# Performance work log

Measured on AMD Instinct MI355X. Metric: run time of the kernel, lower is better.

The kernel has to match this reference:

```python
import jax, jax.numpy as jnp
import numpy as np

N, C, L, NUM_LAYERS = 512, 32, 1024, 3
BN_EPS = 1e-5


def setup_inputs() -> dict:
    key = jax.random.key(0)
    kx, kw, kb, kg, kbe = jax.random.split(key, 5)
    x = jax.random.normal(kx, (N, C, L), dtype=jnp.float32)
    # Per-channel, per-layer Linear weights: (C, num_layers, L_out, L_in)
    W = jax.random.normal(kw, (C, NUM_LAYERS, L, L), dtype=jnp.float32) / np.float32(np.sqrt(L))
    b = 0.01 * jax.random.normal(kb, (C, NUM_LAYERS, L), dtype=jnp.float32)
    # BatchNorm affine params for the num_layers-1 inner BN layers
    gamma = 1.0 + 0.1 * jax.random.normal(kg, (C, NUM_LAYERS - 1, L), dtype=jnp.float32)
    beta = 0.1 * jax.random.normal(kbe, (C, NUM_LAYERS - 1, L), dtype=jnp.float32)
    return {"x": x, "W": W, "b": b, "gamma": gamma, "beta": beta}


def reference(x, W, b, gamma, beta):
    """Fused per-channel MLP head.

    x: (N, C, L). For each channel c, applies num_layers Linear layers with
    ReLU + BatchNorm1d (training-mode batch stats, biased variance) between
    layers. All C channels computed as one batched GEMM per layer.
    """
    h = x
    for i in range(NUM_LAYERS):
        # batched per-channel Linear: (N,C,Lin) x (C,Lout,Lin) -> (N,C,Lout)
        h = jnp.einsum('ncl,cml->ncm', h, W[:, i]) + b[:, i][None]
        if i < NUM_LAYERS - 1:
            h = jax.nn.relu(h)
            # BatchNorm1d over the batch dim N, per (channel, feature)
            mean = jnp.mean(h, axis=0)          # (C, L)
            var = jnp.var(h, axis=0)            # biased variance, matches torch BN
            h = (h - mean) * jax.lax.rsqrt(var + BN_EPS) * gamma[:, i] + beta[:, i]
    return h
```

## Files before the change

kernel.cpp:

```cpp
#include <hip/hip_runtime.h>
#include <hip/hip_bf16.h>

#define NB 512
#define CCH 32
#define LF 1024
#define CL (CCH * LF)
#define BN_EPS 1e-5f

typedef __bf16 bf16x8 __attribute__((ext_vector_type(8)));
typedef __bf16 bf16x4 __attribute__((ext_vector_type(4)));
typedef float f32x4 __attribute__((ext_vector_type(4)));

__device__ __forceinline__ void gload16(const void* g, void* l) {
  auto gp = (const __attribute__((address_space(1))) void*)(uintptr_t)g;
  auto lp = (__attribute__((address_space(3))) void*)(uint32_t)(uintptr_t)l;
  __builtin_amdgcn_global_load_lds(gp, lp, 16, 0, 0);
}

__global__ __launch_bounds__(256) void cvt_x(const float* __restrict__ x,
                                             __bf16* __restrict__ xb) {
  const int c = blockIdx.y;
  const int wv = threadIdx.x >> 6, lane = threadIdx.x & 63;
  const int n0 = blockIdx.x * 8;
#pragma unroll
  for (int rr = 0; rr < 2; ++rr) {
    const int n = n0 + wv * 2 + rr;
    const float* src = x + ((size_t)n * CCH + c) * LF;
    __bf16* dst = xb + ((size_t)c * NB + n) * LF;
#pragma unroll
    for (int j = 0; j < 4; ++j) {
      const int col = (j * 64 + lane) * 4;
      f32x4 v = *(const f32x4*)(src + col);
      bf16x4 o = {(__bf16)v.x, (__bf16)v.y, (__bf16)v.z, (__bf16)v.w};
      *(bf16x4*)(dst + col) = o;
    }
  }
}

template <bool HAS_BN>
__global__ __launch_bounds__(256) void fold_w(
    const float* __restrict__ Wall, const float* __restrict__ ball,
    const float* __restrict__ scale, const float* __restrict__ shift,
    __bf16* __restrict__ Wb, float* __restrict__ bout, int layer) {
  const int c = blockIdx.y;
  const int wv = threadIdx.x >> 6, lane = threadIdx.x & 63;
  const float* Wp = Wall + (size_t)(c * 3 + layer) * LF * LF;
  const float* scl = scale + (size_t)c * LF;
  const float* shf = shift + (size_t)c * LF;
  const int m0 = blockIdx.x * 16 + wv * 4;
#pragma unroll
  for (int rr = 0; rr < 4; ++rr) {
    const int m = m0 + rr;
    const float* wrow = Wp + (size_t)m * LF;
    __bf16* orow = Wb + (size_t)c * LF * LF + (size_t)m * LF;
    float dot = 0.f;
#pragma unroll
    for (int j = 0; j < 4; ++j) {
      const int col = (j * 64 + lane) * 4;
      f32x4 w = *(const f32x4*)(wrow + col);
      if (HAS_BN) {
        f32x4 s = *(const f32x4*)(scl + col);
        f32x4 t = *(const f32x4*)(shf + col);
        dot += w.x * t.x + w.y * t.y + w.z * t.z + w.w * t.w;
        f32x4 wsc = w * s;
        bf16x4 o = {(__bf16)wsc.x, (__bf16)wsc.y, (__bf16)wsc.z, (__bf16)wsc.w};
        *(bf16x4*)(orow + col) = o;
      } else {
        bf16x4 o = {(__bf16)w.x, (__bf16)w.y, (__bf16)w.z, (__bf16)w.w};
        *(bf16x4*)(orow + col) = o;
      }
    }
    if (HAS_BN) {
#pragma unroll
      for (int off = 32; off >= 1; off >>= 1) dot += __shfl_down(dot, off);
    }
    if (lane == 0)
      bout[(size_t)c * LF + m] =
          ball[(size_t)(c * 3 + layer) * LF + m] + (HAS_BN ? dot : 0.f);
  }
}

template <bool RELU, bool OUTBF>
__global__ __launch_bounds__(256, 2) void gemm_k(
    const __bf16* __restrict__ Ab, const __bf16* __restrict__ Wb,
    const float* __restrict__ bf, void* __restrict__ Out) {
  __shared__ __bf16 As[128 * 32];
  __shared__ __bf16 Bs[128 * 32];
  const int tid = threadIdx.x;
  const int c = blockIdx.y;
  const int mtile = blockIdx.x & 3;
  const int ntile = blockIdx.x >> 2;

  const int lane = tid & 63;
  const int wv = tid >> 6;
  const int wm = (wv & 1) * 64;
  const int wn = (wv >> 1) * 64;
  const int l15 = lane & 15;
  const int quad = lane >> 4;

  const int srow = lane >> 2;
  const int skel = (lane & 3) * 8;

  const __bf16* Ag = Ab + (size_t)c * NB * LF +
                     (size_t)(mtile * 128 + wv * 32 + srow) * LF + skel;
  const __bf16* Bg = Wb + (size_t)c * LF * LF +
                     (size_t)(ntile * 128 + wv * 32 + srow) * LF + skel;
  __bf16* Al = &As[(wv * 32) * 32];
  __bf16* Bl = &Bs[(wv * 32) * 32];

  f32x4 acc[4][4] = {};

  for (int kt = 0; kt < LF / 32; ++kt) {
    const int k0 = kt * 32;
    gload16(Ag + k0, Al);
    gload16(Ag + 16 * LF + k0, Al + 16 * 32);
    gload16(Bg + k0, Bl);
    gload16(Bg + 16 * LF + k0, Bl + 16 * 32);
    __syncthreads();

    bf16x8 af[4], bfr[4];
#pragma unroll
    for (int mi = 0; mi < 4; ++mi)
      af[mi] = *(const bf16x8*)&As[(wm + mi * 16 + l15) * 32 + quad * 8];
#pragma unroll
    for (int ni = 0; ni < 4; ++ni)
      bfr[ni] = *(const bf16x8*)&Bs[(wn + ni * 16 + l15) * 32 + quad * 8];
#pragma unroll
    for (int mi = 0; mi < 4; ++mi)
#pragma unroll
      for (int ni = 0; ni < 4; ++ni)
        acc[mi][ni] = __builtin_amdgcn_mfma_f32_16x16x32_bf16(
            af[mi], bfr[ni], acc[mi][ni], 0, 0, 0);
    __syncthreads();
  }

  const float* bias = bf + (size_t)c * LF;
  if (OUTBF) {
    __bf16* outp = (__bf16*)Out + (size_t)c * NB * LF;
#pragma unroll
    for (int ni = 0; ni < 4; ++ni) {
      const int feat = ntile * 128 + wn + ni * 16 + l15;
      const float bvv = bias[feat];
#pragma unroll
      for (int mi = 0; mi < 4; ++mi) {
        const int row0 = mtile * 128 + wm + mi * 16 + quad * 4;
#pragma unroll
        for (int r = 0; r < 4; ++r) {
          float v = acc[mi][ni][r] + bvv;
          if (RELU) v = fmaxf(v, 0.f);
          outp[(size_t)(row0 + r) * LF + feat] = (__bf16)v;
        }
      }
    }
  } else {
    float* outp = (float*)Out + (size_t)c * LF;
#pragma unroll
    for (int ni = 0; ni < 4; ++ni) {
      const int feat = ntile * 128 + wn + ni * 16 + l15;
      const float bvv = bias[feat];
#pragma unroll
      for (int mi = 0; mi < 4; ++mi) {
        const int row0 = mtile * 128 + wm + mi * 16 + quad * 4;
#pragma unroll
        for (int r = 0; r < 4; ++r) {
          float v = acc[mi][ni][r] + bvv;
          if (RELU) v = fmaxf(v, 0.f);
          outp[(size_t)(row0 + r) * CL + feat] = v;
        }
      }
    }
  }
}

__global__ __launch_bounds__(256) void bn_stats(
    const __bf16* __restrict__ H, const float* __restrict__ gamma,
    const float* __restrict__ beta, float* __restrict__ scale,
    float* __restrict__ shift, int bnlayer) {
  __shared__ float s_sum[256], s_sq[256];
  const int tid = threadIdx.x;
  const int f = tid & 63, g = tid >> 6;
  const int c = blockIdx.y;
  const int l = blockIdx.x * 64 + f;
  const __bf16* col = H + (size_t)c * NB * LF + l;
  float sum = 0.f, sq = 0.f;
  for (int n = g; n < NB; n += 4) {
    float v = (float)col[(size_t)n * LF];
    sum += v;
    sq += v * v;
  }
  s_sum[tid] = sum;
  s_sq[tid] = sq;
  __syncthreads();
  if (g == 0) {
    sum = s_sum[f] + s_sum[64 + f] + s_sum[128 + f] + s_sum[192 + f];
    sq = s_sq[f] + s_sq[64 + f] + s_sq[128 + f] + s_sq[192 + f];
    const float mean = sum * (1.f / NB);
    const float var = sq * (1.f / NB) - mean * mean;
    const float rstd = rsqrtf(var + BN_EPS);
    const float ga = gamma[(size_t)(c * 2 + bnlayer) * LF + l];
    const float be = beta[(size_t)(c * 2 + bnlayer) * LF + l];
    const float sc = rstd * ga;
    scale[(size_t)c * LF + l] = sc;
    shift[(size_t)c * LF + l] = be - mean * sc;
  }
}

extern "C" void kernel_launch(void* const* d_in, const int* in_sizes, int n_in,
                              void* d_out, int out_size, void* d_ws,
                              size_t ws_size, hipStream_t stream) {
  const float* x = (const float*)d_in[0];
  const float* W = (const float*)d_in[1];
  const float* b = (const float*)d_in[2];
  const float* gamma = (const float*)d_in[3];
  const float* beta = (const float*)d_in[4];
  float* out = (float*)d_out;

  char* ws = (char*)d_ws;
  float* scale = (float*)ws;  ws += (size_t)CL * 4;
  float* shift = (float*)ws;  ws += (size_t)CL * 4;
  float* bfold = (float*)ws;  ws += (size_t)CL * 4;
  __bf16* xb = (__bf16*)ws;   ws += (size_t)NB * CL * 2;
  __bf16* h1 = (__bf16*)ws;   ws += (size_t)NB * CL * 2;
  __bf16* h2 = (__bf16*)ws;   ws += (size_t)NB * CL * 2;
  __bf16* Wfold = (__bf16*)ws;

  const dim3 blk(256);
  const dim3 ggrid(32, 32);
  const dim3 fgrid(64, 32);
  const dim3 sgrid(16, 32);

  cvt_x<<<fgrid, blk, 0, stream>>>(x, xb);
  fold_w<false><<<fgrid, blk, 0, stream>>>(W, b, scale, shift, Wfold, bfold, 0);
  gemm_k<true, true><<<ggrid, blk, 0, stream>>>(xb, Wfold, bfold, h1);
  bn_stats<<<sgrid, blk, 0, stream>>>(h1, gamma, beta, scale, shift, 0);
  fold_w<true><<<fgrid, blk, 0, stream>>>(W, b, scale, shift, Wfold, bfold, 1);
  gemm_k<true, true><<<ggrid, blk, 0, stream>>>(h1, Wfold, bfold, h2);
  bn_stats<<<sgrid, blk, 0, stream>>>(h2, gamma, beta, scale, shift, 1);
  fold_w<true><<<fgrid, blk, 0, stream>>>(W, b, scale, shift, Wfold, bfold, 2);
  gemm_k<false, false><<<ggrid, blk, 0, stream>>>(h2, Wfold, bfold, out);
}
```

Measured before the change: 867.0 us.

## Apply BatchNorm to activations instead of folding it into weights; convert all weights once

Drops the per-layer weight folding, where BN scale and shift were baked into a bf16 copy of W along with a bias dot product. All three layers' weights are now converted to bf16 in one kernel up front, and BN stats plus normalization are applied directly to the activations, which adds an extra read and write of the activation buffer per layer. The GEMM grid is also remapped to a 1D index that interleaves channels, likely to improve cache locality. This trades the serialized fold-then-GEMM dependency for extra activation traffic and a large up-front weight conversion.

```diff
diff --git a/kernel.cpp b/kernel.cpp
--- a/kernel.cpp
+++ b/kernel.cpp
@@ -37,59 +37,40 @@
   }
 }
 
-template <bool HAS_BN>
-__global__ __launch_bounds__(256) void fold_w(
-    const float* __restrict__ Wall, const float* __restrict__ ball,
-    const float* __restrict__ scale, const float* __restrict__ shift,
-    __bf16* __restrict__ Wb, float* __restrict__ bout, int layer) {
-  const int c = blockIdx.y;
+__global__ __launch_bounds__(256) void cvt_w(const float* __restrict__ Wall,
+                                             __bf16* __restrict__ Wb) {
+  const int slab = blockIdx.y;
   const int wv = threadIdx.x >> 6, lane = threadIdx.x & 63;
-  const float* Wp = Wall + (size_t)(c * 3 + layer) * LF * LF;
-  const float* scl = scale + (size_t)c * LF;
-  const float* shf = shift + (size_t)c * LF;
+  const float* Wp = Wall + (size_t)slab * LF * LF;
+  __bf16* Op = Wb + (size_t)slab * LF * LF;
   const int m0 = blockIdx.x * 16 + wv * 4;
 #pragma unroll
   for (int rr = 0; rr < 4; ++rr) {
     const int m = m0 + rr;
     const float* wrow = Wp + (size_t)m * LF;
-    __bf16* orow = Wb + (size_t)c * LF * LF + (size_t)m * LF;
-    float dot = 0.f;
+    __bf16* orow = Op + (size_t)m * LF;
 #pragma unroll
     for (int j = 0; j < 4; ++j) {
       const int col = (j * 64 + lane) * 4;
       f32x4 w = *(const f32x4*)(wrow + col);
-      if (HAS_BN) {
-        f32x4 s = *(const f32x4*)(scl + col);
-        f32x4 t = *(const f32x4*)(shf + col);
-        dot += w.x * t.x + w.y * t.y + w.z * t.z + w.w * t.w;
-        f32x4 wsc = w * s;
-        bf16x4 o = {(__bf16)wsc.x, (__bf16)wsc.y, (__bf16)wsc.z, (__bf16)wsc.w};
-        *(bf16x4*)(orow + col) = o;
-      } else {
-        bf16x4 o = {(__bf16)w.x, (__bf16)w.y, (__bf16)w.z, (__bf16)w.w};
-        *(bf16x4*)(orow + col) = o;
-      }
-    }
-    if (HAS_BN) {
-#pragma unroll
-      for (int off = 32; off >= 1; off >>= 1) dot += __shfl_down(dot, off);
-    }
-    if (lane == 0)
-      bout[(size_t)c * LF + m] =
-          ball[(size_t)(c * 3 + layer) * LF + m] + (HAS_BN ? dot : 0.f);
+      bf16x4 o = {(__bf16)w.x, (__bf16)w.y, (__bf16)w.z, (__bf16)w.w};
+      *(bf16x4*)(orow + col) = o;
+    }
   }
 }
 
 template <bool RELU, bool OUTBF>
 __global__ __launch_bounds__(256, 2) void gemm_k(
     const __bf16* __restrict__ Ab, const __bf16* __restrict__ Wb,
-    const float* __restrict__ bf, void* __restrict__ Out) {
+    const float* __restrict__ ball, void* __restrict__ Out, int layer) {
   __shared__ __bf16 As[128 * 32];
   __shared__ __bf16 Bs[128 * 32];
   const int tid = threadIdx.x;
-  const int c = blockIdx.y;
-  const int mtile = blockIdx.x & 3;
-  const int ntile = blockIdx.x >> 2;
+  const int bid = blockIdx.x;
+  const int c = (bid & 7) | ((bid >> 8) << 3);
+  const int tile = (bid >> 3) & 31;
+  const int mtile = tile & 3;
+  const int ntile = tile >> 2;
 
   const int lane = tid & 63;
   const int wv = tid >> 6;
@@ -103,7 +84,7 @@
 
   const __bf16* Ag = Ab + (size_t)c * NB * LF +
                      (size_t)(mtile * 128 + wv * 32 + srow) * LF + skel;
-  const __bf16* Bg = Wb + (size_t)c * LF * LF +
+  const __bf16* Bg = Wb + (size_t)(c * 3 + layer) * LF * LF +
                      (size_t)(ntile * 128 + wv * 32 + srow) * LF + skel;
   __bf16* Al = &As[(wv * 32) * 32];
   __bf16* Bl = &Bs[(wv * 32) * 32];
@@ -134,7 +115,7 @@
     __syncthreads();
   }
 
-  const float* bias = bf + (size_t)c * LF;
+  const float* bias = ball + (size_t)(c * 3 + layer) * LF;
   if (OUTBF) {
     __bf16* outp = (__bf16*)Out + (size_t)c * NB * LF;
 #pragma unroll
@@ -172,11 +153,11 @@
   }
 }
 
-__global__ __launch_bounds__(256) void bn_stats(
+__global__ __launch_bounds__(256) void bn_norm(
     const __bf16* __restrict__ H, const float* __restrict__ gamma,
-    const float* __restrict__ beta, float* __restrict__ scale,
-    float* __restrict__ shift, int bnlayer) {
+    const float* __restrict__ beta, __bf16* __restrict__ Hn, int bnlayer) {
   __shared__ float s_sum[256], s_sq[256];
+  __shared__ float s_sc[64], s_sh[64];
   const int tid = threadIdx.x;
   const int f = tid & 63, g = tid >> 6;
   const int c = blockIdx.y;
@@ -200,8 +181,16 @@
     const float ga = gamma[(size_t)(c * 2 + bnlayer) * LF + l];
     const float be = beta[(size_t)(c * 2 + bnlayer) * LF + l];
     const float sc = rstd * ga;
-    scale[(size_t)c * LF + l] = sc;
-    shift[(size_t)c * LF + l] = be - mean * sc;
+    s_sc[f] = sc;
+    s_sh[f] = be - mean * sc;
+  }
+  __syncthreads();
+  const float sc = s_sc[f];
+  const float sh = s_sh[f];
+  __bf16* ocol = Hn + (size_t)c * NB * LF + l;
+  for (int n = g; n < NB; n += 4) {
+    float v = (float)col[(size_t)n * LF];
+    ocol[(size_t)n * LF] = (__bf16)(v * sc + sh);
   }
 }
 
@@ -216,26 +205,24 @@
   float* out = (float*)d_out;
 
   char* ws = (char*)d_ws;
-  float* scale = (float*)ws;  ws += (size_t)CL * 4;
-  float* shift = (float*)ws;  ws += (size_t)CL * 4;
-  float* bfold = (float*)ws;  ws += (size_t)CL * 4;
   __bf16* xb = (__bf16*)ws;   ws += (size_t)NB * CL * 2;
   __bf16* h1 = (__bf16*)ws;   ws += (size_t)NB * CL * 2;
+  __bf16* h1n = (__bf16*)ws;  ws += (size_t)NB * CL * 2;
   __bf16* h2 = (__bf16*)ws;   ws += (size_t)NB * CL * 2;
-  __bf16* Wfold = (__bf16*)ws;
+  __bf16* h2n = (__bf16*)ws;  ws += (size_t)NB * CL * 2;
+  __bf16* Wb = (__bf16*)ws;
 
   const dim3 blk(256);
-  const dim3 ggrid(32, 32);
-  const dim3 fgrid(64, 32);
+  const dim3 cgrid(64, 32);
+  const dim3 wgrid(64, 96);
   const dim3 sgrid(16, 32);
-
-  cvt_x<<<fgrid, blk, 0, stream>>>(x, xb);
-  fold_w<false><<<fgrid, blk, 0, stream>>>(W, b, scale, shift, Wfold, bfold, 0);
-  gemm_k<true, true><<<ggrid, blk, 0, stream>>>(xb, Wfold, bfold, h1);
-  bn_stats<<<sgrid, blk, 0, stream>>>(h1, gamma, beta, scale, shift, 0);
-  fold_w<true><<<fgrid, blk, 0, stream>>>(W, b, scale, shift, Wfold, bfold, 1);
-  gemm_k<true, true><<<ggrid, blk, 0, stream>>>(h1, Wfold, bfold, h2);
-  bn_stats<<<sgrid, blk, 0, stream>>>(h2, gamma, beta, scale, shift, 1);
-  fold_w<true><<<fgrid, blk, 0, stream>>>(W, b, scale, shift, Wfold, bfold, 2);
-  gemm_k<false, false><<<ggrid, blk, 0, stream>>>(h2, Wfold, bfold, out);
-}
+  const int ggrid = 1024;
+
+  cvt_x<<<cgrid, blk, 0, stream>>>(x, xb);
+  cvt_w<<<wgrid, blk, 0, stream>>>(W, Wb);
+  gemm_k<true, true><<<ggrid, blk, 0, stream>>>(xb, Wb, b, h1, 0);
+  bn_norm<<<sgrid, blk, 0, stream>>>(h1, gamma, beta, h1n, 0);
+  gemm_k<true, true><<<ggrid, blk, 0, stream>>>(h1n, Wb, b, h2, 1);
+  bn_norm<<<sgrid, blk, 0, stream>>>(h2, gamma, beta, h2n, 1);
+  gemm_k<false, false><<<ggrid, blk, 0, stream>>>(h2n, Wb, b, out, 2);
+}
```

After: 863.6 us. About the same (-0.4%).
